# Performance work log

Measured on AMD Instinct MI355X. Metric: run time of the kernel, lower is better.

The kernel has to match this reference:

```python
import jax, jax.numpy as jnp
import numpy as np

WS = 7           # window size
N = WS * WS      # tokens per window = 49
C = 128          # embed dim
H = 4            # heads
HD = C // H      # head dim = 32
NW = 64          # num windows (mask leading dim)
B = 4096         # total windows = outer_batch * NW


def _relative_indexes():
    ch = np.arange(WS)
    cw = np.arange(WS)
    coords = np.stack(np.meshgrid(ch, cw, indexing='ij')).reshape(2, -1)  # [2, N]
    rel = coords[:, :, None] - coords[:, None, :]                          # [2, N, N]
    rel = rel.transpose(1, 2, 0)
    rel[:, :, 0] += WS - 1
    rel[:, :, 1] += WS - 1
    rel[:, :, 0] *= 2 * WS - 1
    return jnp.asarray(rel.sum(-1), dtype=jnp.int32)                       # [N, N]


def setup_inputs() -> dict:
    key = jax.random.key(0)
    ks = jax.random.split(key, 10)
    s = 0.02
    return {
        'query': jax.random.normal(ks[0], (B, N, C), jnp.float32),
        'source': jax.random.normal(ks[1], (B, N, C), jnp.float32),
        'mask': jnp.zeros((NW, N, N), jnp.float32),
        'q_w': jax.random.normal(ks[2], (C, C), jnp.float32) * s,
        'q_b': jnp.zeros((C,), jnp.float32),
        'kv_w': jax.random.normal(ks[3], (C, 2 * C), jnp.float32) * s,
        'kv_b': jnp.zeros((2 * C,), jnp.float32),
        'proj_w': jax.random.normal(ks[4], (C, C), jnp.float32) * s,
        'proj_b': jnp.zeros((C,), jnp.float32),
        'bias_table': jax.random.normal(ks[5], ((2 * WS - 1) ** 2, H), jnp.float32) * s,
        'rel_idx': _relative_indexes(),
    }


def reference(query, source, mask, q_w, q_b, kv_w, kv_b, proj_w, proj_b, bias_table, rel_idx):
    scale = HD ** -0.5
    q = query @ q_w + q_b                       # [B, N, C]
    kv = source @ kv_w + kv_b                   # [B, N, 2C]
    k, v = kv[..., :C], kv[..., C:]
    # [B, N, H, HD] -> [B, H, N, HD]
    q = q.reshape(B, N, H, HD).transpose(0, 2, 1, 3) * scale
    k = k.reshape(B, N, H, HD).transpose(0, 2, 1, 3)
    v = v.reshape(B, N, H, HD).transpose(0, 2, 1, 3)
    attn = jnp.einsum('bhnd,bhmd->bhnm', q, k)  # [B, H, N, N]
    # gathered relative positional bias: [1, H, N, N]
    bias = bias_table[rel_idx.reshape(-1)].reshape(N, N, H).transpose(2, 0, 1)[None]
    attn = attn + bias
    # mask: [NW, N, N] broadcast over outer batch and heads
    attn = attn.reshape(-1, NW, H, N, N) + mask[None, :, None]
    attn = attn.reshape(B, H, N, N)
    attn = jax.nn.softmax(attn, axis=-1)
    x = jnp.einsum('bhnm,bhmd->bnhd', attn, v).reshape(B, N, C)
    return x @ proj_w + proj_b
```

## Files before the change

### kernel.cpp

```cpp
#include <hip/hip_runtime.h>

#define NN 49
#define CC 128
#define HH 4
#define NWIN 64
#define BB 4096
#define QSCALE 0.17677669529663687f

typedef __attribute__((ext_vector_type(8))) short bf16x8;
typedef __attribute__((ext_vector_type(4))) float f32x4;
typedef unsigned short u16;
typedef unsigned int u32;

__device__ __forceinline__ u16 f2b(float f) {
    u32 x = __float_as_uint(f);
    return (u16)((x + 0x7fffu + ((x >> 16) & 1u)) >> 16);
}
__device__ __forceinline__ float b2f(u16 u) { return __uint_as_float(((u32)u) << 16); }
__device__ __forceinline__ uint2 pack4(float a, float b, float c, float d) {
    uint2 r;
    r.x = (u32)f2b(a) | ((u32)f2b(b) << 16);
    r.y = (u32)f2b(c) | ((u32)f2b(d) << 16);
    return r;
}
__device__ __forceinline__ f32x4 mfma16(bf16x8 a, bf16x8 b, f32x4 c) {
    return __builtin_amdgcn_mfma_f32_16x16x32_bf16(a, b, c, 0, 0, 0);
}
__device__ __forceinline__ char* adr256(u16* base, int row, int byte) {
    return (char*)base + row * 256 + (byte ^ ((row & 7) << 4));
}
__device__ __forceinline__ char* adr128(u16* base, int row, int byte) {
    return (char*)base + row * 128 + (byte ^ ((row & 7) << 4));
}

__global__ void prep_cbt(const float* __restrict__ bias_table, const int* __restrict__ rel_idx,
                         const float* __restrict__ mask, u16* __restrict__ cbt) {
    int idx = blockIdx.x * blockDim.x + threadIdx.x;
    int m = idx & 63, i = (idx >> 6) & 63, h = (idx >> 12) & 3, wv = idx >> 14;
    if (wv >= NWIN) return;
    float v = -1e9f;
    if (m < NN && i < NN)
        v = bias_table[rel_idx[i * NN + m] * HH + h] + mask[(wv * NN + i) * NN + m];
    cbt[idx] = f2b(v);
}

__global__ void prep_w(const float* __restrict__ qw, const float* __restrict__ qb,
                       const float* __restrict__ kvw, const float* __restrict__ pjw,
                       u16* __restrict__ qwp, u16* __restrict__ kvwp,
                       u16* __restrict__ pjwp, float* __restrict__ qbs) {
    int idx = blockIdx.x * blockDim.x + threadIdx.x;
    if (idx < 16384) {
        int i = idx & 7, lane = (idx >> 3) & 63, kt = (idx >> 9) & 3, nt = idx >> 11;
        int k = 32 * kt + 8 * (lane >> 4) + i, n = 16 * nt + (lane & 15);
        qwp[idx] = f2b(qw[k * CC + n] * QSCALE);
    } else if (idx < 49152) {
        int j = idx - 16384;
        int i = j & 7, lane = (j >> 3) & 63, kt = (j >> 9) & 3, nt = j >> 11;
        int k = 32 * kt + 8 * (lane >> 4) + i, n = 16 * nt + (lane & 15);
        kvwp[j] = f2b(kvw[k * 2 * CC + n]);
    } else if (idx < 65536) {
        int j = idx - 49152;
        int i = j & 7, lane = (j >> 3) & 63, kt = (j >> 9) & 3, nt = j >> 11;
        int k = 32 * kt + 8 * (lane >> 4) + i, n = 16 * nt + (lane & 15);
        pjwp[j] = f2b(pjw[k * CC + n]);
    } else if (idx < 65664) {
        int j = idx - 65536;
        qbs[j] = qb[j] * QSCALE;
    }
}

__global__ __launch_bounds__(256, 3)
void wmha_main(const float* __restrict__ query, const float* __restrict__ source,
               const u16* __restrict__ qwp, const u16* __restrict__ kvwp,
               const u16* __restrict__ pjwp, const float* __restrict__ qbs,
               const float* __restrict__ kv_b, const float* __restrict__ proj_b,
               const u16* __restrict__ cbt, float* __restrict__ out) {
    __shared__ u16 lds[24576];
    u16* R0 = lds;
    u16* R1 = lds + 8192;
    u16* R2 = lds + 16384;
    const int t = threadIdx.x;
    const int b = blockIdx.x;
    const int w = t >> 6, lane = t & 63;
    const int lq = lane & 15, qd = lane >> 4;

    {
        const int row = t >> 2, qu = t & 3;
        const size_t gbase = (size_t)b * NN * CC + row * CC + qu * 32;
        #pragma unroll
        for (int j = 0; j < 4; ++j) {
            bf16x8 vq = {0,0,0,0,0,0,0,0}, vs = {0,0,0,0,0,0,0,0};
            if (row < NN) {
                const float4* q4 = (const float4*)(query + gbase) + 2 * j;
                const float4* s4 = (const float4*)(source + gbase) + 2 * j;
                float4 a0 = q4[0], a1 = q4[1], c0 = s4[0], c1 = s4[1];
                vq[0]=(short)f2b(a0.x); vq[1]=(short)f2b(a0.y); vq[2]=(short)f2b(a0.z); vq[3]=(short)f2b(a0.w);
                vq[4]=(short)f2b(a1.x); vq[5]=(short)f2b(a1.y); vq[6]=(short)f2b(a1.z); vq[7]=(short)f2b(a1.w);
                vs[0]=(short)f2b(c0.x); vs[1]=(short)f2b(c0.y); vs[2]=(short)f2b(c0.z); vs[3]=(short)f2b(c0.w);
                vs[4]=(short)f2b(c1.x); vs[5]=(short)f2b(c1.y); vs[6]=(short)f2b(c1.z); vs[7]=(short)f2b(c1.w);
            }
            *(bf16x8*)adr256(R0, row, qu * 64 + 16 * j) = vq;
            *(bf16x8*)adr256(R2, row, qu * 64 + 16 * j) = vs;
        }
    }
    bf16x8 bwq[2][4];
    #pragma unroll
    for (int n2 = 0; n2 < 2; ++n2)
        #pragma unroll
        for (int kt = 0; kt < 4; ++kt)
            bwq[n2][kt] = *(const bf16x8*)(qwp + (((w + 4 * n2) * 4 + kt) * 64 + lane) * 8);
    __syncthreads();

    {
        f32x4 acc[4][2] = {};
        __builtin_amdgcn_s_setprio(1);
        #pragma unroll
        for (int mt = 0; mt < 4; ++mt) {
            bf16x8 a[4];
            #pragma unroll
            for (int kt = 0; kt < 4; ++kt)
                a[kt] = *(const bf16x8*)adr256(R0, mt * 16 + lq, kt * 64 + qd * 16);
            #pragma unroll
            for (int n2 = 0; n2 < 2; ++n2)
                #pragma unroll
                for (int kt = 0; kt < 4; ++kt)
                    acc[mt][n2] = mfma16(a[kt], bwq[n2][kt], acc[mt][n2]);
        }
        __builtin_amdgcn_s_setprio(0);
        #pragma unroll
        for (int n2 = 0; n2 < 2; ++n2) {
            const int col = 16 * (w + 4 * n2) + lq;
            const float bias = qbs[col];
            #pragma unroll
            for (int mt = 0; mt < 4; ++mt)
                #pragma unroll
                for (int r = 0; r < 4; ++r) {
                    const int row = mt * 16 + qd * 4 + r;
                    *(u16*)adr256(R1, row, 2 * col) = f2b(acc[mt][n2][r] + bias);
                }
        }
    }
    __syncthreads();

    {
        bf16x8 bw[2][4];
        #pragma unroll
        for (int n2 = 0; n2 < 2; ++n2)
            #pragma unroll
            for (int kt = 0; kt < 4; ++kt)
                bw[n2][kt] = *(const bf16x8*)(kvwp + (((w + 4 * n2) * 4 + kt) * 64 + lane) * 8);
        f32x4 acc[4][2] = {};
        __builtin_amdgcn_s_setprio(1);
        #pragma unroll
        for (int mt = 0; mt < 4; ++mt) {
            bf16x8 a[4];
            #pragma unroll
            for (int kt = 0; kt < 4; ++kt)
                a[kt] = *(const bf16x8*)adr256(R2, mt * 16 + lq, kt * 64 + qd * 16);
            #pragma unroll
            for (int n2 = 0; n2 < 2; ++n2)
                #pragma unroll
                for (int kt = 0; kt < 4; ++kt)
                    acc[mt][n2] = mfma16(a[kt], bw[n2][kt], acc[mt][n2]);
        }
        __builtin_amdgcn_s_setprio(0);
        #pragma unroll
        for (int n2 = 0; n2 < 2; ++n2) {
            const int col = 16 * (w + 4 * n2) + lq;
            const float bias = kv_b[col];
            #pragma unroll
            for (int mt = 0; mt < 4; ++mt)
                #pragma unroll
                for (int r = 0; r < 4; ++r) {
                    const int row = mt * 16 + qd * 4 + r;
                    *(u16*)adr256(R0, row, 2 * col) = f2b(acc[mt][n2][r] + bias);
                }
        }
    }

    {
        bf16x8 bw[2][4];
        #pragma unroll
        for (int n2 = 0; n2 < 2; ++n2)
            #pragma unroll
            for (int kt = 0; kt < 4; ++kt)
                bw[n2][kt] = *(const bf16x8*)(kvwp + (((w + 8 + 4 * n2) * 4 + kt) * 64 + lane) * 8);
        f32x4 acc[4][2] = {};
        __builtin_amdgcn_s_setprio(1);
        #pragma unroll
        for (int mt = 0; mt < 4; ++mt) {
            bf16x8 a[4];
            #pragma unroll
            for (int kt = 0; kt < 4; ++kt)
                a[kt] = *(const bf16x8*)adr256(R2, mt * 16 + lq, kt * 64 + qd * 16);
            #pragma unroll
            for (int n2 = 0; n2 < 2; ++n2)
                #pragma unroll
                for (int kt = 0; kt < 4; ++kt)
                    acc[mt][n2] = mfma16(a[kt], bw[n2][kt], acc[mt][n2]);
        }
        __builtin_amdgcn_s_setprio(0);
        __syncthreads();
        #pragma unroll
        for (int n2 = 0; n2 < 2; ++n2) {
            const int dim = 16 * w + 64 * n2 + lq;
            const float bias = kv_b[CC + dim];
            #pragma unroll
            for (int mt = 0; mt < 4; ++mt) {
                uint2 pk = pack4(acc[mt][n2][0] + bias, acc[mt][n2][1] + bias,
                                 acc[mt][n2][2] + bias, acc[mt][n2][3] + bias);
                *(uint2*)adr128(R2, dim, 2 * (mt * 16 + qd * 4)) = pk;
            }
        }
    }

    const int h = w;
    f32x4 s[4][4];
    {
        bf16x8 kf[4];
        #pragma unroll
        for (int a = 0; a < 4; ++a)
            kf[a] = *(const bf16x8*)adr256(R0, a * 16 + lq, h * 64 + qd * 16);
        __builtin_amdgcn_s_setprio(1);
        #pragma unroll
        for (int bq = 0; bq < 4; ++bq) {
            bf16x8 qf = *(const bf16x8*)adr256(R1, bq * 16 + lq, h * 64 + qd * 16);
            f32x4 z = {0.f, 0.f, 0.f, 0.f};
            #pragma unroll
            for (int a = 0; a < 4; ++a)
                s[bq][a] = mfma16(kf[a], qf, z);
        }
        __builtin_amdgcn_s_setprio(0);
    }
    __syncthreads();

    {
        bf16x8 vf[2][2];
        #pragma unroll
        for (int dt = 0; dt < 2; ++dt)
            #pragma unroll
            for (int kt = 0; kt < 2; ++kt)
                vf[dt][kt] = *(const bf16x8*)adr128(R2, h * 32 + dt * 16 + lq, kt * 64 + qd * 16);
        u16* pb = R0 + w * 1024;
        const u16* cbb = cbt + ((size_t)((b & (NWIN - 1)) * HH + h) << 12);
        #pragma unroll
        for (int bq = 0; bq < 4; ++bq) {
            uint2 cb2[4];
            #pragma unroll
            for (int a = 0; a < 4; ++a)
                cb2[a] = *(const uint2*)(cbb + (bq * 16 + lq) * 64 + a * 16 + qd * 4);
            #pragma unroll
            for (int a = 0; a < 4; ++a) {
                s[bq][a][0] += b2f((u16)(cb2[a].x & 0xffffu));
                s[bq][a][1] += b2f((u16)(cb2[a].x >> 16));
                s[bq][a][2] += b2f((u16)(cb2[a].y & 0xffffu));
                s[bq][a][3] += b2f((u16)(cb2[a].y >> 16));
            }
            float m0 = s[bq][0][0];
            #pragma unroll
            for (int a = 0; a < 4; ++a)
                #pragma unroll
                for (int r = 0; r < 4; ++r) m0 = fmaxf(m0, s[bq][a][r]);
            m0 = fmaxf(m0, __shfl_xor(m0, 16));
            m0 = fmaxf(m0, __shfl_xor(m0, 32));
            uint2 pk[4];
            float sm = 0.f;
            #pragma unroll
            for (int a = 0; a < 4; ++a) {
                float p0 = __expf(s[bq][a][0] - m0), p1 = __expf(s[bq][a][1] - m0);
                float p2 = __expf(s[bq][a][2] - m0), p3 = __expf(s[bq][a][3] - m0);
                pk[a] = pack4(p0, p1, p2, p3);
                sm += b2f((u16)pk[a].x) + b2f((u16)(pk[a].x >> 16))
                    + b2f((u16)pk[a].y) + b2f((u16)(pk[a].y >> 16));
            }
            sm += __shfl_xor(sm, 16);
            sm += __shfl_xor(sm, 32);
            const float inv = 1.f / sm;
            #pragma unroll
            for (int a = 0; a < 4; ++a)
                *(uint2*)adr128(pb, lq, 32 * a + 8 * qd) = pk[a];
            asm volatile("s_waitcnt lgkmcnt(0)" ::: "memory");
            __builtin_amdgcn_sched_barrier(0);
            f32x4 o[2] = {{0.f,0.f,0.f,0.f},{0.f,0.f,0.f,0.f}};
            __builtin_amdgcn_s_setprio(1);
            #pragma unroll
            for (int kt = 0; kt < 2; ++kt) {
                bf16x8 pf = *(const bf16x8*)adr128(pb, lq, 64 * kt + 16 * qd);
                #pragma unroll
                for (int dt = 0; dt < 2; ++dt)
                    o[dt] = mfma16(vf[dt][kt], pf, o[dt]);
            }
            __builtin_amdgcn_s_setprio(0);
            __builtin_amdgcn_sched_barrier(0);
            #pragma unroll
            for (int dt = 0; dt < 2; ++dt) {
                uint2 px = pack4(o[dt][0] * inv, o[dt][1] * inv,
                                 o[dt][2] * inv, o[dt][3] * inv);
                *(uint2*)adr256(R1, bq * 16 + lq, 64 * h + 32 * dt + 8 * qd) = px;
            }
        }
    }

    {
        bf16x8 bw[2][4];
        #pragma unroll
        for (int n2 = 0; n2 < 2; ++n2)
            #pragma unroll
            for (int kt = 0; kt < 4; ++kt)
                bw[n2][kt] = *(const bf16x8*)(pjwp + (((w + 4 * n2) * 4 + kt) * 64 + lane) * 8);
        __syncthreads();
        f32x4 acc[4][2] = {};
        __builtin_amdgcn_s_setprio(1);
        #pragma unroll
        for (int mt = 0; mt < 4; ++mt) {
            bf16x8 a[4];
            #pragma unroll
            for (int kt = 0; kt < 4; ++kt)
                a[kt] = *(const bf16x8*)adr256(R1, mt * 16 + lq, kt * 64 + qd * 16);
            #pragma unroll
            for (int n2 = 0; n2 < 2; ++n2)
                #pragma unroll
                for (int kt = 0; kt < 4; ++kt)
                    acc[mt][n2] = mfma16(a[kt], bw[n2][kt], acc[mt][n2]);
        }
        __builtin_amdgcn_s_setprio(0);
        float* outb = out + (size_t)b * NN * CC;
        #pragma unroll
        for (int n2 = 0; n2 < 2; ++n2) {
            const int col = 16 * (w + 4 * n2) + lq;
            const float bias = proj_b[col];
            #pragma unroll
            for (int mt = 0; mt < 4; ++mt)
                #pragma unroll
                for (int r = 0; r < 4; ++r) {
                    const int row = mt * 16 + qd * 4 + r;
                    if (row < NN) outb[row * CC + col] = acc[mt][n2][r] + bias;
                }
        }
    }
}

extern "C" void kernel_launch(void* const* d_in, const int* in_sizes, int n_in,
                              void* d_out, int out_size, void* d_ws, size_t ws_size,
                              hipStream_t stream) {
    const float* query      = (const float*)d_in[0];
    const float* source     = (const float*)d_in[1];
    const float* mask       = (const float*)d_in[2];
    const float* q_w        = (const float*)d_in[3];
    const float* q_b        = (const float*)d_in[4];
    const float* kv_w       = (const float*)d_in[5];
    const float* kv_b       = (const float*)d_in[6];
    const float* proj_w     = (const float*)d_in[7];
    const float* proj_b     = (const float*)d_in[8];
    const float* bias_table = (const float*)d_in[9];
    const int*   rel_idx    = (const int*)d_in[10];
    float* out = (float*)d_out;

    u16* cbt   = (u16*)d_ws;
    u16* qwp   = cbt + 1048576;
    u16* kvwp  = qwp + 16384;
    u16* pjwp  = kvwp + 32768;
    float* qbs = (float*)(pjwp + 16384);

    prep_cbt<<<4096, 256, 0, stream>>>(bias_table, rel_idx, mask, cbt);
    prep_w<<<257, 256, 0, stream>>>(q_w, q_b, kv_w, proj_w, qwp, kvwp, pjwp, qbs);
    wmha_main<<<BB, 256, 0, stream>>>(query, source, qwp, kvwp, pjwp, qbs,
                                      kv_b, proj_b, cbt, out);
}
```

Measured before the change: 125.3 us.

## Double the waves per window block and split row tiles and heads across them

```diff
diff --git a/kernel.cpp b/kernel.cpp
--- a/kernel.cpp
+++ b/kernel.cpp
@@ -1,4 +1,5 @@
 #include <hip/hip_runtime.h>
+#include <hip/hip_bf16.h>
 
 #define NN 49
 #define CC 128
@@ -13,8 +14,8 @@
 typedef unsigned int u32;
 
 __device__ __forceinline__ u16 f2b(float f) {
-    u32 x = __float_as_uint(f);
-    return (u16)((x + 0x7fffu + ((x >> 16) & 1u)) >> 16);
+    __hip_bfloat16 h = __float2bfloat16(f);
+    return __builtin_bit_cast(u16, h);
 }
 __device__ __forceinline__ float b2f(u16 u) { return __uint_as_float(((u32)u) << 16); }
 __device__ __forceinline__ uint2 pack4(float a, float b, float c, float d) {
@@ -69,7 +70,7 @@
     }
 }
 
-__global__ __launch_bounds__(256, 3)
+__global__ __launch_bounds__(512, 6)
 void wmha_main(const float* __restrict__ query, const float* __restrict__ source,
                const u16* __restrict__ qwp, const u16* __restrict__ kvwp,
                const u16* __restrict__ pjwp, const float* __restrict__ qbs,
@@ -83,24 +84,28 @@
     const int b = blockIdx.x;
     const int w = t >> 6, lane = t & 63;
     const int lq = lane & 15, qd = lane >> 4;
-
-    {
-        const int row = t >> 2, qu = t & 3;
-        const size_t gbase = (size_t)b * NN * CC + row * CC + qu * 32;
-        #pragma unroll
-        for (int j = 0; j < 4; ++j) {
+    const int mw = w >> 2;
+    const int nw = w & 3;
+    const int h = w >> 1;
+    const int half = w & 1;
+
+    {
+        const int row = t >> 3, qu = t & 7;
+        const size_t gbase = (size_t)b * NN * CC + row * CC + qu * 8;
+        #pragma unroll
+        for (int j = 0; j < 2; ++j) {
             bf16x8 vq = {0,0,0,0,0,0,0,0}, vs = {0,0,0,0,0,0,0,0};
             if (row < NN) {
-                const float4* q4 = (const float4*)(query + gbase) + 2 * j;
-                const float4* s4 = (const float4*)(source + gbase) + 2 * j;
+                const float4* q4 = (const float4*)(query + gbase) + 16 * j;
+                const float4* s4 = (const float4*)(source + gbase) + 16 * j;
                 float4 a0 = q4[0], a1 = q4[1], c0 = s4[0], c1 = s4[1];
                 vq[0]=(short)f2b(a0.x); vq[1]=(short)f2b(a0.y); vq[2]=(short)f2b(a0.z); vq[3]=(short)f2b(a0.w);
                 vq[4]=(short)f2b(a1.x); vq[5]=(short)f2b(a1.y); vq[6]=(short)f2b(a1.z); vq[7]=(short)f2b(a1.w);
                 vs[0]=(short)f2b(c0.x); vs[1]=(short)f2b(c0.y); vs[2]=(short)f2b(c0.z); vs[3]=(short)f2b(c0.w);
                 vs[4]=(short)f2b(c1.x); vs[5]=(short)f2b(c1.y); vs[6]=(short)f2b(c1.z); vs[7]=(short)f2b(c1.w);
             }
-            *(bf16x8*)adr256(R0, row, qu * 64 + 16 * j) = vq;
-            *(bf16x8*)adr256(R2, row, qu * 64 + 16 * j) = vs;
+            *(bf16x8*)adr256(R0, row, qu * 16 + 128 * j) = vq;
+            *(bf16x8*)adr256(R2, row, qu * 16 + 128 * j) = vs;
         }
     }
     bf16x8 bwq[2][4];
@@ -108,35 +113,36 @@
     for (int n2 = 0; n2 < 2; ++n2)
         #pragma unroll
         for (int kt = 0; kt < 4; ++kt)
-            bwq[n2][kt] = *(const bf16x8*)(qwp + (((w + 4 * n2) * 4 + kt) * 64 + lane) * 8);
+            bwq[n2][kt] = *(const bf16x8*)(qwp + (((nw + 4 * n2) * 4 + kt) * 64 + lane) * 8);
     __syncthreads();
 
     {
-        f32x4 acc[4][2] = {};
-        __builtin_amdgcn_s_setprio(1);
-        #pragma unroll
-        for (int mt = 0; mt < 4; ++mt) {
-            bf16x8 a[4];
-            #pragma unroll
-            for (int kt = 0; kt < 4; ++kt)
-                a[kt] = *(const bf16x8*)adr256(R0, mt * 16 + lq, kt * 64 + qd * 16);
+        bf16x8 a[2][4];
+        #pragma unroll
+        for (int m2 = 0; m2 < 2; ++m2)
+            #pragma unroll
+            for (int kt = 0; kt < 4; ++kt)
+                a[m2][kt] = *(const bf16x8*)adr256(R0, (2 * mw + m2) * 16 + lq, kt * 64 + qd * 16);
+        f32x4 acc[2][2] = {};
+        __builtin_amdgcn_s_setprio(1);
+        #pragma unroll
+        for (int m2 = 0; m2 < 2; ++m2)
             #pragma unroll
             for (int n2 = 0; n2 < 2; ++n2)
                 #pragma unroll
                 for (int kt = 0; kt < 4; ++kt)
-                    acc[mt][n2] = mfma16(a[kt], bwq[n2][kt], acc[mt][n2]);
-        }
+                    acc[m2][n2] = mfma16(a[m2][kt], bwq[n2][kt], acc[m2][n2]);
         __builtin_amdgcn_s_setprio(0);
         #pragma unroll
         for (int n2 = 0; n2 < 2; ++n2) {
-            const int col = 16 * (w + 4 * n2) + lq;
+            const int col = 16 * (nw + 4 * n2) + lq;
             const float bias = qbs[col];
             #pragma unroll
-            for (int mt = 0; mt < 4; ++mt)
+            for (int m2 = 0; m2 < 2; ++m2)
                 #pragma unroll
                 for (int r = 0; r < 4; ++r) {
-                    const int row = mt * 16 + qd * 4 + r;
-                    *(u16*)adr256(R1, row, 2 * col) = f2b(acc[mt][n2][r] + bias);
+                    const int row = (2 * mw + m2) * 16 + qd * 4 + r;
+                    *(u16*)adr256(R1, row, 2 * col) = f2b(acc[m2][n2][r] + bias);
                 }
         }
     }
@@ -148,32 +154,33 @@
         for (int n2 = 0; n2 < 2; ++n2)
             #pragma unroll
             for (int kt = 0; kt < 4; ++kt)
-                bw[n2][kt] = *(const bf16x8*)(kvwp + (((w + 4 * n2) * 4 + kt) * 64 + lane) * 8);
-        f32x4 acc[4][2] = {};
-        __builtin_amdgcn_s_setprio(1);
-        #pragma unroll
-        for (int mt = 0; mt < 4; ++mt) {
-            bf16x8 a[4];
-            #pragma unroll
-            for (int kt = 0; kt < 4; ++kt)
-                a[kt] = *(const bf16x8*)adr256(R2, mt * 16 + lq, kt * 64 + qd * 16);
+                bw[n2][kt] = *(const bf16x8*)(kvwp + (((nw + 4 * n2) * 4 + kt) * 64 + lane) * 8);
+        bf16x8 a[2][4];
+        #pragma unroll
+        for (int m2 = 0; m2 < 2; ++m2)
+            #pragma unroll
+            for (int kt = 0; kt < 4; ++kt)
+                a[m2][kt] = *(const bf16x8*)adr256(R2, (2 * mw + m2) * 16 + lq, kt * 64 + qd * 16);
+        f32x4 acc[2][2] = {};
+        __builtin_amdgcn_s_setprio(1);
+        #pragma unroll
+        for (int m2 = 0; m2 < 2; ++m2)
             #pragma unroll
             for (int n2 = 0; n2 < 2; ++n2)
                 #pragma unroll
                 for (int kt = 0; kt < 4; ++kt)
-                    acc[mt][n2] = mfma16(a[kt], bw[n2][kt], acc[mt][n2]);
-        }
+                    acc[m2][n2] = mfma16(a[m2][kt], bw[n2][kt], acc[m2][n2]);
         __builtin_amdgcn_s_setprio(0);
         #pragma unroll
         for (int n2 = 0; n2 < 2; ++n2) {
-            const int col = 16 * (w + 4 * n2) + lq;
+            const int col = 16 * (nw + 4 * n2) + lq;
             const float bias = kv_b[col];
             #pragma unroll
-            for (int mt = 0; mt < 4; ++mt)
+            for (int m2 = 0; m2 < 2; ++m2)
                 #pragma unroll
                 for (int r = 0; r < 4; ++r) {
-                    const int row = mt * 16 + qd * 4 + r;
-                    *(u16*)adr256(R0, row, 2 * col) = f2b(acc[mt][n2][r] + bias);
+                    const int row = (2 * mw + m2) * 16 + qd * 4 + r;
+                    *(u16*)adr256(R0, row, 2 * col) = f2b(acc[m2][n2][r] + bias);
                 }
         }
     }
@@ -184,51 +191,53 @@
         for (int n2 = 0; n2 < 2; ++n2)
             #pragma unroll
             for (int kt = 0; kt < 4; ++kt)
-                bw[n2][kt] = *(const bf16x8*)(kvwp + (((w + 8 + 4 * n2) * 4 + kt) * 64 + lane) * 8);
-        f32x4 acc[4][2] = {};
-        __builtin_amdgcn_s_setprio(1);
-        #pragma unroll
-        for (int mt = 0; mt < 4; ++mt) {
-            bf16x8 a[4];
-            #pragma unroll
-            for (int kt = 0; kt < 4; ++kt)
-                a[kt] = *(const bf16x8*)adr256(R2, mt * 16 + lq, kt * 64 + qd * 16);
+                bw[n2][kt] = *(const bf16x8*)(kvwp + (((8 + nw + 4 * n2) * 4 + kt) * 64 + lane) * 8);
+        bf16x8 a[2][4];
+        #pragma unroll
+        for (int m2 = 0; m2 < 2; ++m2)
+            #pragma unroll
+            for (int kt = 0; kt < 4; ++kt)
+                a[m2][kt] = *(const bf16x8*)adr256(R2, (2 * mw + m2) * 16 + lq, kt * 64 + qd * 16);
+        f32x4 acc[2][2] = {};
+        __builtin_amdgcn_s_setprio(1);
+        #pragma unroll
+        for (int m2 = 0; m2 < 2; ++m2)
             #pragma unroll
             for (int n2 = 0; n2 < 2; ++n2)
                 #pragma unroll
                 for (int kt = 0; kt < 4; ++kt)
-                    acc[mt][n2] = mfma16(a[kt], bw[n2][kt], acc[mt][n2]);
-        }
+                    acc[m2][n2] = mfma16(a[m2][kt], bw[n2][kt], acc[m2][n2]);
         __builtin_amdgcn_s_setprio(0);
         __syncthreads();
         #pragma unroll
         for (int n2 = 0; n2 < 2; ++n2) {
-            const int dim = 16 * w + 64 * n2 + lq;
+            const int dim = 16 * (nw + 4 * n2) + lq;
             const float bias = kv_b[CC + dim];
             #pragma unroll
-            for (int mt = 0; mt < 4; ++mt) {
-                uint2 pk = pack4(acc[mt][n2][0] + bias, acc[mt][n2][1] + bias,
-                                 acc[mt][n2][2] + bias, acc[mt][n2][3] + bias);
-                *(uint2*)adr128(R2, dim, 2 * (mt * 16 + qd * 4)) = pk;
-            }
-        }
-    }
-
-    const int h = w;
-    f32x4 s[4][4];
-    {
-        bf16x8 kf[4];
+            for (int m2 = 0; m2 < 2; ++m2) {
+                uint2 pk = pack4(acc[m2][n2][0] + bias, acc[m2][n2][1] + bias,
+                                 acc[m2][n2][2] + bias, acc[m2][n2][3] + bias);
+                *(uint2*)adr128(R2, dim, 2 * ((2 * mw + m2) * 16 + qd * 4)) = pk;
+            }
+        }
+    }
+
+    f32x4 s[2][4];
+    {
+        bf16x8 kf[4], qf[2];
         #pragma unroll
         for (int a = 0; a < 4; ++a)
             kf[a] = *(const bf16x8*)adr256(R0, a * 16 + lq, h * 64 + qd * 16);
-        __builtin_amdgcn_s_setprio(1);
-        #pragma unroll
-        for (int bq = 0; bq < 4; ++bq) {
-            bf16x8 qf = *(const bf16x8*)adr256(R1, bq * 16 + lq, h * 64 + qd * 16);
+        #pragma unroll
+        for (int i = 0; i < 2; ++i)
+            qf[i] = *(const bf16x8*)adr256(R1, (2 * half + i) * 16 + lq, h * 64 + qd * 16);
+        __builtin_amdgcn_s_setprio(1);
+        #pragma unroll
+        for (int i = 0; i < 2; ++i) {
             f32x4 z = {0.f, 0.f, 0.f, 0.f};
             #pragma unroll
             for (int a = 0; a < 4; ++a)
-                s[bq][a] = mfma16(kf[a], qf, z);
+                s[i][a] = mfma16(kf[a], qf[i], z);
         }
         __builtin_amdgcn_s_setprio(0);
     }
@@ -244,31 +253,32 @@
         u16* pb = R0 + w * 1024;
         const u16* cbb = cbt + ((size_t)((b & (NWIN - 1)) * HH + h) << 12);
         #pragma unroll
-        for (int bq = 0; bq < 4; ++bq) {
+        for (int i = 0; i < 2; ++i) {
+            const int bq = 2 * half + i;
             uint2 cb2[4];
             #pragma unroll
             for (int a = 0; a < 4; ++a)
                 cb2[a] = *(const uint2*)(cbb + (bq * 16 + lq) * 64 + a * 16 + qd * 4);
             #pragma unroll
             for (int a = 0; a < 4; ++a) {
-                s[bq][a][0] += b2f((u16)(cb2[a].x & 0xffffu));
-                s[bq][a][1] += b2f((u16)(cb2[a].x >> 16));
-                s[bq][a][2] += b2f((u16)(cb2[a].y & 0xffffu));
-                s[bq][a][3] += b2f((u16)(cb2[a].y >> 16));
-            }
-            float m0 = s[bq][0][0];
+                s[i][a][0] += b2f((u16)(cb2[a].x & 0xffffu));
+                s[i][a][1] += b2f((u16)(cb2[a].x >> 16));
+                s[i][a][2] += b2f((u16)(cb2[a].y & 0xffffu));
+                s[i][a][3] += b2f((u16)(cb2[a].y >> 16));
+            }
+            float m0 = s[i][0][0];
             #pragma unroll
             for (int a = 0; a < 4; ++a)
                 #pragma unroll
-                for (int r = 0; r < 4; ++r) m0 = fmaxf(m0, s[bq][a][r]);
+                for (int r = 0; r < 4; ++r) m0 = fmaxf(m0, s[i][a][r]);
             m0 = fmaxf(m0, __shfl_xor(m0, 16));
             m0 = fmaxf(m0, __shfl_xor(m0, 32));
             uint2 pk[4];
             float sm = 0.f;
             #pragma unroll
             for (int a = 0; a < 4; ++a) {
-                float p0 = __expf(s[bq][a][0] - m0), p1 = __expf(s[bq][a][1] - m0);
-                float p2 = __expf(s[bq][a][2] - m0), p3 = __expf(s[bq][a][3] - m0);
+                float p0 = __expf(s[i][a][0] - m0), p1 = __expf(s[i][a][1] - m0);
+                float p2 = __expf(s[i][a][2] - m0), p3 = __expf(s[i][a][3] - m0);
                 pk[a] = pack4(p0, p1, p2, p3);
                 sm += b2f((u16)pk[a].x) + b2f((u16)(pk[a].x >> 16))
                     + b2f((u16)pk[a].y) + b2f((u16)(pk[a].y >> 16));
@@ -307,34 +317,35 @@
         for (int n2 = 0; n2 < 2; ++n2)
             #pragma unroll
             for (int kt = 0; kt < 4; ++kt)
-                bw[n2][kt] = *(const bf16x8*)(pjwp + (((w + 4 * n2) * 4 + kt) * 64 + lane) * 8);
+                bw[n2][kt] = *(const bf16x8*)(pjwp + (((nw + 4 * n2) * 4 + kt) * 64 + lane) * 8);
         __syncthreads();
-        f32x4 acc[4][2] = {};
-        __builtin_amdgcn_s_setprio(1);
-        #pragma unroll
-        for (int mt = 0; mt < 4; ++mt) {
-            bf16x8 a[4];
-            #pragma unroll
-            for (int kt = 0; kt < 4; ++kt)
-                a[kt] = *(const bf16x8*)adr256(R1, mt * 16 + lq, kt * 64 + qd * 16);
+        bf16x8 a[2][4];
+        #pragma unroll
+        for (int m2 = 0; m2 < 2; ++m2)
+            #pragma unroll
+            for (int kt = 0; kt < 4; ++kt)
+                a[m2][kt] = *(const bf16x8*)adr256(R1, (2 * mw + m2) * 16 + lq, kt * 64 + qd * 16);
+        f32x4 acc[2][2] = {};
+        __builtin_amdgcn_s_setprio(1);
+        #pragma unroll
+        for (int m2 = 0; m2 < 2; ++m2)
             #pragma unroll
             for (int n2 = 0; n2 < 2; ++n2)
                 #pragma unroll
                 for (int kt = 0; kt < 4; ++kt)
-                    acc[mt][n2] = mfma16(a[kt], bw[n2][kt], acc[mt][n2]);
-        }
+                    acc[m2][n2] = mfma16(a[m2][kt], bw[n2][kt], acc[m2][n2]);
         __builtin_amdgcn_s_setprio(0);
         float* outb = out + (size_t)b * NN * CC;
         #pragma unroll
         for (int n2 = 0; n2 < 2; ++n2) {
-            const int col = 16 * (w + 4 * n2) + lq;
+            const int col = 16 * (nw + 4 * n2) + lq;
             const float bias = proj_b[col];
             #pragma unroll
-            for (int mt = 0; mt < 4; ++mt)
+            for (int m2 = 0; m2 < 2; ++m2)
                 #pragma unroll
                 for (int r = 0; r < 4; ++r) {
-                    const int row = mt * 16 + qd * 4 + r;
-                    if (row < NN) outb[row * CC + col] = acc[mt][n2][r] + bias;
+                    const int row = (2 * mw + m2) * 16 + qd * 4 + r;
+                    if (row < NN) outb[row * CC + col] = acc[m2][n2][r] + bias;
                 }
         }
     }
@@ -364,6 +375,6 @@
 
     prep_cbt<<<4096, 256, 0, stream>>>(bias_table, rel_idx, mask, cbt);
     prep_w<<<257, 256, 0, stream>>>(q_w, q_b, kv_w, proj_w, qwp, kvwp, pjwp, qbs);
-    wmha_main<<<BB, 256, 0, stream>>>(query, source, qwp, kvwp, pjwp, qbs,
+    wmha_main<<<BB, 512, 0, stream>>>(query, source, qwp, kvwp, pjwp, qbs,
                                       kv_b, proj_b, cbt, out);
 }
```

Measured after the change: 214.7 us. +71.4%, slower.
